# Performance work log

Measured on AMD Instinct MI355X. Metric: run time of the kernel, lower is better.

Reference implementation:

```python
import jax, jax.numpy as jnp
import numpy as np


def _relative_position_index(ws: int) -> np.ndarray:
    # Matches torch meshgrid (ij) construction in _init_relative_positions.
    coords = np.stack(np.meshgrid(np.arange(ws), np.arange(ws), indexing='ij'), axis=0).reshape(2, -1)  # [2, ws*ws]
    rel = coords[:, :, None] - coords[:, None, :]          # [2, N, N]
    rel = rel.transpose(1, 2, 0).copy()                    # [N, N, 2]
    rel[:, :, 0] += ws - 1
    rel[:, :, 1] += ws - 1
    rel[:, :, 0] *= 2 * ws - 1
    return rel.sum(-1)                                     # [N, N] int


def setup_inputs() -> dict:
    key = jax.random.key(0)
    ks = jax.random.split(key, 6)
    B, N, C, H, WS = 4096, 49, 512, 16, 7
    x = jax.random.normal(ks[0], (B, N, C), dtype=jnp.float32)
    w_qkv = jax.random.normal(ks[1], (C, 3 * C), dtype=jnp.float32) * (C ** -0.5)
    b_qkv = jax.random.normal(ks[2], (3 * C,), dtype=jnp.float32) * 0.02
    w_proj = jax.random.normal(ks[3], (C, C), dtype=jnp.float32) * (C ** -0.5)
    b_proj = jax.random.normal(ks[4], (C,), dtype=jnp.float32) * 0.02
    bias_table = jax.random.normal(ks[5], ((2 * WS - 1) ** 2, H), dtype=jnp.float32) * 0.02
    return {"x": x, "w_qkv": w_qkv, "b_qkv": b_qkv, "w_proj": w_proj,
            "b_proj": b_proj, "bias_table": bias_table,
            "num_heads": H, "window_size": WS}


def reference(x, w_qkv, b_qkv, w_proj, b_proj, bias_table, num_heads, window_size):
    B, N, C = x.shape
    hd = C // num_heads
    qkv = (x @ w_qkv + b_qkv).reshape(B, N, 3, num_heads, hd)
    q, k, v = (qkv[:, :, i].transpose(0, 2, 1, 3) for i in range(3))  # each [B, H, N, hd]
    # NOTE: scale uses full channel dim C (as in source), not head_dim.
    attn = jnp.einsum('bhnd,bhmd->bhnm', q, k) * (C ** -0.5)          # [B, H, N, N]
    idx = _relative_position_index(window_size)                        # [N, N] static
    rel_bias = bias_table[idx].transpose(2, 0, 1)                      # [H, N, N]
    attn = jax.nn.softmax(attn + rel_bias[None], axis=-1)
    out = jnp.einsum('bhnm,bhmd->bhnd', attn, v)                       # [B, H, N, hd]
    out = out.transpose(0, 2, 1, 3).reshape(B, N, C)
    return out @ w_proj + b_proj
```

## Files before the change

### kernel.cpp

```cpp
#include <hip/hip_runtime.h>
#include <hip/hip_bf16.h>

typedef __attribute__((ext_vector_type(8))) short bf16x8;
typedef __attribute__((ext_vector_type(4))) float f32x4;

#define DEVI __device__ __forceinline__

DEVI short f2bf(float f) {
  union { float f; unsigned u; } v; v.f = f;
  unsigned r = v.u + 0x7FFFu + ((v.u >> 16) & 1u);
  return (short)(r >> 16);
}

DEVI void gl16(const void* g, void* l) {
  __builtin_amdgcn_global_load_lds((const __attribute__((address_space(1))) unsigned*)g,
                                   (__attribute__((address_space(3))) unsigned*)l,
                                   16, 0, 0);
}

DEVI float exp2a(float x) { float r; asm("v_exp_f32 %0, %1" : "=v"(r) : "v"(x)); return r; }

DEVI unsigned pk2(float lo, float hi) {
  union { __hip_bfloat162 h; unsigned u; } v;
  float2 f; f.x = lo; f.y = hi;
  v.h = __float22bfloat162_rn(f);
  return v.u;
}

union U8 { unsigned u[4]; bf16x8 v; };
DEVI bf16x8 mk8(unsigned a, unsigned b, unsigned c, unsigned d) {
  U8 x; x.u[0]=a; x.u[1]=b; x.u[2]=c; x.u[3]=d; return x.v;
}


__global__ __launch_bounds__(256) void conv_x_k(const float* __restrict__ x,
                                                short* __restrict__ xb) {
  long i = (long)blockIdx.x * 256 + threadIdx.x;
  const float4* xf = (const float4*)x;
  float4 a = xf[i * 2], c = xf[i * 2 + 1];
  bf16x8 r;
  r[0] = f2bf(a.x); r[1] = f2bf(a.y); r[2] = f2bf(a.z); r[3] = f2bf(a.w);
  r[4] = f2bf(c.x); r[5] = f2bf(c.y); r[6] = f2bf(c.z); r[7] = f2bf(c.w);
  *(bf16x8*)(xb + i * 8) = r;
}

__global__ __launch_bounds__(256) void conv_wT_k(const float* __restrict__ w,
                                                 short* __restrict__ wT, int Ncols) {
  int i = blockIdx.x * 256 + threadIdx.x;
  if (i >= Ncols * 512) return;
  int n = i >> 9, k = i & 511;
  wT[i] = f2bf(w[k * Ncols + n]);
}

__global__ __launch_bounds__(256) void fill_biasT(const float* __restrict__ btab,
                                                  float* __restrict__ biasT) {
  int i = blockIdx.x * 256 + threadIdx.x;
  int h = i >> 12, m = (i >> 6) & 63, n = i & 63;
  float v;
  if (m >= 49) {
    v = -1e30f;
  } else {
    int nn = n > 48 ? 48 : n;
    int ni = nn / 7, nj = nn - ni * 7;
    int mi = m / 7,  mj = m - mi * 7;
    int idx = (ni - mi + 6) * 13 + (nj - mj + 6);
    v = btab[idx * 16 + h] * 1.4426950408889634f;
  }
  biasT[i] = v;
}


template <int EPI>
__global__ __launch_bounds__(256, 2)
void gemm128(const short* __restrict__ A, const short* __restrict__ Bt,
             const float* __restrict__ bias, void* __restrict__ outp, int ctiles) {
  __shared__ short As[4096];
  __shared__ short Bs[4096];

  const int nwg = gridDim.x;
  const int w = blockIdx.x;
  const int chunk = nwg >> 3;
  const int tid = (w & 7) * chunk + (w >> 3);
  const int rt = tid / ctiles, ct = tid % ctiles;
  const long m0 = (long)rt * 128;
  const int n0 = ct * 128;

  const int t = threadIdx.x;
  const int lane = t & 63;
  const int wv = t >> 6;
  const int wm = wv >> 1, wn = wv & 1;
  const int l15 = lane & 15, g = lane >> 4;

  const int rA0 = t >> 2;
  const int cSw = (t & 3) ^ ((t >> 3) & 3);
  const short* Ag0 = A + (m0 + rA0) * 512 + cSw * 8;
  const short* Ag1 = A + (m0 + rA0 + 64) * 512 + cSw * 8;
  const short* Bg0 = Bt + (long)(n0 + rA0) * 512 + cSw * 8;
  const short* Bg1 = Bt + (long)(n0 + rA0 + 64) * 512 + cSw * 8;
  short* Al0 = As + t * 8;
  short* Al1 = As + (t + 256) * 8;
  short* Bl0 = Bs + t * 8;
  short* Bl1 = Bs + (t + 256) * 8;

  const int xl = (l15 >> 1) & 3;
  const short* aRd = As + (wm * 64 + l15) * 32 + (g ^ xl) * 8;
  const short* bRd = Bs + (wn * 64 + l15) * 32 + (g ^ xl) * 8;

  f32x4 acc[4][4] = {};

  for (int kk = 0; kk < 512; kk += 32) {
    __syncthreads();
    gl16(Ag0 + kk, Al0);
    gl16(Ag1 + kk, Al1);
    gl16(Bg0 + kk, Bl0);
    gl16(Bg1 + kk, Bl1);
    __syncthreads();
    bf16x8 a[4], b[4];
#pragma unroll
    for (int i = 0; i < 4; ++i) a[i] = *(const bf16x8*)(aRd + i * 512);
#pragma unroll
    for (int j = 0; j < 4; ++j) b[j] = *(const bf16x8*)(bRd + j * 512);
#pragma unroll
    for (int i = 0; i < 4; ++i)
#pragma unroll
      for (int j = 0; j < 4; ++j)
        acc[i][j] = __builtin_amdgcn_mfma_f32_16x16x32_bf16(a[i], b[j], acc[i][j], 0, 0, 0);
  }

  if (EPI == 0) {
    short* qkv = (short*)outp;
#pragma unroll
    for (int i = 0; i < 4; ++i)
#pragma unroll
      for (int r = 0; r < 4; ++r) {
        int row = (int)m0 + wm * 64 + i * 16 + g * 4 + r;
        int b = row / 49, n = row - b * 49;
#pragma unroll
        for (int j = 0; j < 4; ++j) {
          int col = n0 + wn * 64 + j * 16 + l15;
          float val = acc[i][j][r] + bias[col];
          int ii = col >> 9, h = (col >> 5) & 15, d = col & 31;
          qkv[(long)((b * 16 + h) * 3 + ii) * 1568 + n * 32 + d] = f2bf(val);
        }
      }
  } else {
    float* out = (float*)outp;
#pragma unroll
    for (int i = 0; i < 4; ++i)
#pragma unroll
      for (int r = 0; r < 4; ++r) {
        long row = m0 + wm * 64 + i * 16 + g * 4 + r;
#pragma unroll
        for (int j = 0; j < 4; ++j) {
          int col = n0 + wn * 64 + j * 16 + l15;
          out[row * 512 + col] = acc[i][j][r] + bias[col];
        }
      }
  }
}


__global__ __launch_bounds__(256, 3)
void attn49(const short* __restrict__ qkvb, const float* __restrict__ biasT,
            short* __restrict__ ao) {
  const int t = threadIdx.x, lane = t & 63, wv = t >> 6;
  const int l15 = lane & 15, g = lane >> 4, g4 = g * 4;
  const int b = blockIdx.x >> 2;
  const int h = (blockIdx.x & 3) * 4 + wv;

  const short* qb = qkvb + (long)(b * 16 + h) * 3 * 1568;
  const short* kb = qb + 1568;
  const short* vb = kb + 1568;

  bf16x8 qf[4], kf[4];
#pragma unroll
  for (int i = 0; i < 4; ++i) {
    int row = i * 16 + l15; row = row > 48 ? 48 : row;
    kf[i] = *(const bf16x8*)(kb + row * 32 + g * 8);
    qf[i] = *(const bf16x8*)(qb + row * 32 + g * 8);
  }

  bf16x8 vf[2][2];
#pragma unroll
  for (int kt = 0; kt < 2; ++kt)
#pragma unroll
    for (int hi = 0; hi < 2; ++hi)
#pragma unroll
      for (int r = 0; r < 4; ++r) {
        int m = kt * 32 + hi * 16 + g4 + r;
        m = m > 48 ? 48 : m;
#pragma unroll
        for (int dt = 0; dt < 2; ++dt)
          vf[kt][dt][hi * 4 + r] = vb[m * 32 + dt * 16 + l15];
      }

  f32x4 s[4][4] = {};
#pragma unroll
  for (int i = 0; i < 4; ++i)
#pragma unroll
    for (int j = 0; j < 4; ++j)
      s[i][j] = __builtin_amdgcn_mfma_f32_16x16x32_bf16(kf[i], qf[j], s[i][j], 0, 0, 0);

  const float* biasH = biasT + h * 4096;
  float sum[4] = {0.f, 0.f, 0.f, 0.f};
#pragma unroll
  for (int i = 0; i < 4; ++i)
#pragma unroll
    for (int r = 0; r < 4; ++r) {
      int m = i * 16 + g4 + r;
      const float* bp = biasH + m * 64 + l15;
#pragma unroll
      for (int j = 0; j < 4; ++j) {
        float p = exp2a(fmaf(s[i][j][r], 0.06375871f, bp[j * 16]));
        s[i][j][r] = p;
        sum[j] += p;
      }
    }
#pragma unroll
  for (int j = 0; j < 4; ++j) {
    sum[j] += __shfl_xor(sum[j], 16);
    sum[j] += __shfl_xor(sum[j], 32);
    sum[j] = 1.f / sum[j];
  }

  unsigned pk[4][4][2];
#pragma unroll
  for (int j = 0; j < 4; ++j)
#pragma unroll
    for (int i = 0; i < 4; ++i) {
      pk[j][i][0] = pk2(s[i][j][0] * sum[j], s[i][j][1] * sum[j]);
      pk[j][i][1] = pk2(s[i][j][2] * sum[j], s[i][j][3] * sum[j]);
    }

  f32x4 o[4][2] = {};
#pragma unroll
  for (int j = 0; j < 4; ++j) {
    bf16x8 a0 = mk8(pk[j][0][0], pk[j][0][1], pk[j][1][0], pk[j][1][1]);
    bf16x8 a1 = mk8(pk[j][2][0], pk[j][2][1], pk[j][3][0], pk[j][3][1]);
    o[j][0] = __builtin_amdgcn_mfma_f32_16x16x32_bf16(a0, vf[0][0], o[j][0], 0, 0, 0);
    o[j][0] = __builtin_amdgcn_mfma_f32_16x16x32_bf16(a1, vf[1][0], o[j][0], 0, 0, 0);
    o[j][1] = __builtin_amdgcn_mfma_f32_16x16x32_bf16(a0, vf[0][1], o[j][1], 0, 0, 0);
    o[j][1] = __builtin_amdgcn_mfma_f32_16x16x32_bf16(a1, vf[1][1], o[j][1], 0, 0, 0);
  }

#pragma unroll
  for (int j = 0; j < 4; ++j)
#pragma unroll
    for (int r = 0; r < 4; ++r) {
      int n = j * 16 + g4 + r;
      if (n < 49) {
        long off = ((long)b * 49 + n) * 512 + h * 32 + l15;
        ao[off]      = f2bf(o[j][0][r]);
        ao[off + 16] = f2bf(o[j][1][r]);
      }
    }
}


extern "C" void kernel_launch(void* const* d_in, const int* in_sizes, int n_in,
                              void* d_out, int out_size, void* d_ws, size_t ws_size,
                              hipStream_t stream) {
  (void)in_sizes; (void)n_in; (void)out_size; (void)ws_size;
  const float* x      = (const float*)d_in[0];
  const float* w_qkv  = (const float*)d_in[1];
  const float* b_qkv  = (const float*)d_in[2];
  const float* w_proj = (const float*)d_in[3];
  const float* b_proj = (const float*)d_in[4];
  const float* btab   = (const float*)d_in[5];

  char* ws = (char*)d_ws;
  short* xb  = (short*)ws;
  short* wqT = (short*)(ws + 205520896L);
  short* wpT = (short*)(ws + 205520896L + 1572864L);
  short* qkv = (short*)(ws + 205520896L + 1572864L + 524288L);
  short* ao  = xb;
  float* biasT = (float*)wqT;

  conv_x_k <<<50176, 256, 0, stream>>>(x, xb);
  conv_wT_k<<<3072, 256, 0, stream>>>(w_qkv, wqT, 1536);
  conv_wT_k<<<1024, 256, 0, stream>>>(w_proj, wpT, 512);
  gemm128<0><<<18816, 256, 0, stream>>>(xb, wqT, b_qkv, (void*)qkv, 12);
  fill_biasT<<<256, 256, 0, stream>>>(btab, biasT);
  attn49   <<<16384, 256, 0, stream>>>(qkv, biasT, ao);
  gemm128<1><<<6272, 256, 0, stream>>>(ao, wpT, b_proj, d_out, 4);
}
```

Baseline: 949.4 us.

## Use 256x256 GEMM tiles with double-buffered LDS and 512-thread blocks

Replaces the 128x128 single-buffered GEMM with a 256x256 tile computed by 8 waves, K-step 64, and a double-buffered 128KB LDS ring whose next-tile global-to-LDS loads are issued between MFMA batches. This aims to raise arithmetic intensity per LDS byte and hide load latency behind compute, removing one barrier per k-step. The cost is higher register pressure (32 accumulators per lane) and a large LDS footprint that limits occupancy, and the launch counts must match the new tile count.

```diff
diff --git a/kernel.cpp b/kernel.cpp
--- a/kernel.cpp
+++ b/kernel.cpp
@@ -71,74 +71,103 @@
 
 
 template <int EPI>
-__global__ __launch_bounds__(256, 2)
-void gemm128(const short* __restrict__ A, const short* __restrict__ Bt,
+__global__ __launch_bounds__(512, 2)
+void gemm256(const short* __restrict__ A, const short* __restrict__ Bt,
              const float* __restrict__ bias, void* __restrict__ outp, int ctiles) {
-  __shared__ short As[4096];
-  __shared__ short Bs[4096];
+  __shared__ short Ls[65536];
 
   const int nwg = gridDim.x;
   const int w = blockIdx.x;
   const int chunk = nwg >> 3;
   const int tid = (w & 7) * chunk + (w >> 3);
   const int rt = tid / ctiles, ct = tid % ctiles;
-  const long m0 = (long)rt * 128;
-  const int n0 = ct * 128;
+  const long m0 = (long)rt * 256;
+  const int n0 = ct * 256;
 
   const int t = threadIdx.x;
   const int lane = t & 63;
   const int wv = t >> 6;
-  const int wm = wv >> 1, wn = wv & 1;
+  const int wr = wv >> 2;
+  const int wc = wv & 3;
   const int l15 = lane & 15, g = lane >> 4;
 
-  const int rA0 = t >> 2;
-  const int cSw = (t & 3) ^ ((t >> 3) & 3);
-  const short* Ag0 = A + (m0 + rA0) * 512 + cSw * 8;
-  const short* Ag1 = A + (m0 + rA0 + 64) * 512 + cSw * 8;
-  const short* Bg0 = Bt + (long)(n0 + rA0) * 512 + cSw * 8;
-  const short* Bg1 = Bt + (long)(n0 + rA0 + 64) * 512 + cSw * 8;
-  short* Al0 = As + t * 8;
-  short* Al1 = As + (t + 256) * 8;
-  short* Bl0 = Bs + t * 8;
-  short* Bl1 = Bs + (t + 256) * 8;
-
-  const int xl = (l15 >> 1) & 3;
-  const short* aRd = As + (wm * 64 + l15) * 32 + (g ^ xl) * 8;
-  const short* bRd = Bs + (wn * 64 + l15) * 32 + (g ^ xl) * 8;
-
-  f32x4 acc[4][4] = {};
-
-  for (int kk = 0; kk < 512; kk += 32) {
+  const int srow = t >> 3;
+  const int gch = (t & 7) ^ (srow & 7);
+  const short* Ag = A + (m0 + srow) * 512 + gch * 8;
+  const short* Bg = Bt + (long)(n0 + srow) * 512 + gch * 8;
+
+  const int x7 = l15 & 7;
+  const int c0 = (g ^ x7) * 8;
+  const int c1 = ((4 + g) ^ x7) * 8;
+  const int rA64 = (wr * 128 + l15) * 64;
+  const int rB64 = (wc * 64 + l15) * 64 + 16384;
+
+  f32x4 acc[8][4] = {};
+
+  {
+    short* Ad = Ls + t * 8;
+    short* Bd = Ls + 16384 + t * 8;
+#pragma unroll
+    for (int s2 = 0; s2 < 4; ++s2) {
+      gl16(Ag + s2 * 32768, Ad + s2 * 4096);
+      gl16(Bg + s2 * 32768, Bd + s2 * 4096);
+    }
+  }
+  __syncthreads();
+
+  for (int kt = 0; kt < 8; ++kt) {
+    const int cur = kt & 1;
+    const short* Ab = Ls + cur * 32768;
+    short* Ad = Ls + (cur ^ 1) * 32768 + t * 8;
+    short* Bd = Ad + 16384;
+    const short* Agk = Ag + (kt + 1) * 64;
+    const short* Bgk = Bg + (kt + 1) * 64;
+
+    bf16x8 af[8], bf[4];
+
+#pragma unroll
+    for (int mf = 0; mf < 8; ++mf) af[mf] = *(const bf16x8*)(Ab + rA64 + mf * 1024 + c0);
+#pragma unroll
+    for (int nf = 0; nf < 4; ++nf) bf[nf] = *(const bf16x8*)(Ab + rB64 + nf * 1024 + c0);
+    if (kt < 7) {
+#pragma unroll
+      for (int s2 = 0; s2 < 4; ++s2) gl16(Agk + s2 * 32768, Ad + s2 * 4096);
+    }
+#pragma unroll
+    for (int mf = 0; mf < 8; ++mf)
+#pragma unroll
+      for (int nf = 0; nf < 4; ++nf)
+        acc[mf][nf] = __builtin_amdgcn_mfma_f32_16x16x32_bf16(af[mf], bf[nf], acc[mf][nf], 0, 0, 0);
+
+#pragma unroll
+    for (int mf = 0; mf < 8; ++mf) af[mf] = *(const bf16x8*)(Ab + rA64 + mf * 1024 + c1);
+#pragma unroll
+    for (int nf = 0; nf < 4; ++nf) bf[nf] = *(const bf16x8*)(Ab + rB64 + nf * 1024 + c1);
+    if (kt < 7) {
+#pragma unroll
+      for (int s2 = 0; s2 < 4; ++s2) gl16(Bgk + s2 * 32768, Bd + s2 * 4096);
+    }
+#pragma unroll
+    for (int mf = 0; mf < 8; ++mf)
+#pragma unroll
+      for (int nf = 0; nf < 4; ++nf)
+        acc[mf][nf] = __builtin_amdgcn_mfma_f32_16x16x32_bf16(af[mf], bf[nf], acc[mf][nf], 0, 0, 0);
+
     __syncthreads();
-    gl16(Ag0 + kk, Al0);
-    gl16(Ag1 + kk, Al1);
-    gl16(Bg0 + kk, Bl0);
-    gl16(Bg1 + kk, Bl1);
-    __syncthreads();
-    bf16x8 a[4], b[4];
-#pragma unroll
-    for (int i = 0; i < 4; ++i) a[i] = *(const bf16x8*)(aRd + i * 512);
-#pragma unroll
-    for (int j = 0; j < 4; ++j) b[j] = *(const bf16x8*)(bRd + j * 512);
-#pragma unroll
-    for (int i = 0; i < 4; ++i)
-#pragma unroll
-      for (int j = 0; j < 4; ++j)
-        acc[i][j] = __builtin_amdgcn_mfma_f32_16x16x32_bf16(a[i], b[j], acc[i][j], 0, 0, 0);
   }
 
   if (EPI == 0) {
     short* qkv = (short*)outp;
 #pragma unroll
-    for (int i = 0; i < 4; ++i)
+    for (int mf = 0; mf < 8; ++mf)
 #pragma unroll
       for (int r = 0; r < 4; ++r) {
-        int row = (int)m0 + wm * 64 + i * 16 + g * 4 + r;
+        int row = (int)m0 + wr * 128 + mf * 16 + g * 4 + r;
         int b = row / 49, n = row - b * 49;
 #pragma unroll
-        for (int j = 0; j < 4; ++j) {
-          int col = n0 + wn * 64 + j * 16 + l15;
-          float val = acc[i][j][r] + bias[col];
+        for (int nf = 0; nf < 4; ++nf) {
+          int col = n0 + wc * 64 + nf * 16 + l15;
+          float val = acc[mf][nf][r] + bias[col];
           int ii = col >> 9, h = (col >> 5) & 15, d = col & 31;
           qkv[(long)((b * 16 + h) * 3 + ii) * 1568 + n * 32 + d] = f2bf(val);
         }
@@ -146,14 +175,14 @@
   } else {
     float* out = (float*)outp;
 #pragma unroll
-    for (int i = 0; i < 4; ++i)
+    for (int mf = 0; mf < 8; ++mf)
 #pragma unroll
       for (int r = 0; r < 4; ++r) {
-        long row = m0 + wm * 64 + i * 16 + g * 4 + r;
-#pragma unroll
-        for (int j = 0; j < 4; ++j) {
-          int col = n0 + wn * 64 + j * 16 + l15;
-          out[row * 512 + col] = acc[i][j][r] + bias[col];
+        long row = m0 + wr * 128 + mf * 16 + g * 4 + r;
+#pragma unroll
+        for (int nf = 0; nf < 4; ++nf) {
+          int col = n0 + wc * 64 + nf * 16 + l15;
+          out[row * 512 + col] = acc[mf][nf][r] + bias[col];
         }
       }
   }
@@ -279,8 +308,8 @@
   conv_x_k <<<50176, 256, 0, stream>>>(x, xb);
   conv_wT_k<<<3072, 256, 0, stream>>>(w_qkv, wqT, 1536);
   conv_wT_k<<<1024, 256, 0, stream>>>(w_proj, wpT, 512);
-  gemm128<0><<<18816, 256, 0, stream>>>(xb, wqT, b_qkv, (void*)qkv, 12);
+  gemm256<0><<<4704, 512, 0, stream>>>(xb, wqT, b_qkv, (void*)qkv, 6);
   fill_biasT<<<256, 256, 0, stream>>>(btab, biasT);
   attn49   <<<16384, 256, 0, stream>>>(qkv, biasT, ao);
-  gemm128<1><<<6272, 256, 0, stream>>>(ao, wpT, b_proj, d_out, 4);
-}
+  gemm256<1><<<1568, 512, 0, stream>>>(ao, wpT, b_proj, d_out, 2);
+}
```

Measured after the change: 958.0 us. About the same (+0.9%).
